# Optimization experiments

Measured on AMD Instinct MI355X. Metric: run time of the kernel, lower is better.

Reference implementation:

```python
import jax, jax.numpy as jnp
import numpy as np

N_NODES = 50000
N_EDGES = 800000
D = 64
N_GRAPHS = 512
N_LAYERS = 3
HID_FC = 64
N_CLASSES = 10


def setup_inputs() -> dict:
    key = jax.random.key(0)
    ks = jax.random.split(key, 12)
    s = 1.0 / np.sqrt(D)
    x = jax.random.normal(ks[0], (N_NODES, D), dtype=jnp.float32)
    edge_index = jax.random.randint(ks[1], (2, N_EDGES), 0, N_NODES, dtype=jnp.int32)
    batch = jnp.sort(jax.random.randint(ks[2], (N_NODES,), 0, N_GRAPHS, dtype=jnp.int32))
    convW1 = jax.random.normal(ks[3], (N_LAYERS, D, D), dtype=jnp.float32) * s
    convb1 = jax.random.normal(ks[4], (N_LAYERS, D), dtype=jnp.float32) * 0.01
    convW2 = jax.random.normal(ks[5], (N_LAYERS, D, D), dtype=jnp.float32) * s
    convb2 = jax.random.normal(ks[6], (N_LAYERS, D), dtype=jnp.float32) * 0.01
    fcW1 = jax.random.normal(ks[7], (D, HID_FC), dtype=jnp.float32) * s
    fcb1 = jax.random.normal(ks[8], (HID_FC,), dtype=jnp.float32) * 0.01
    fcW2 = jax.random.normal(ks[9], (HID_FC, N_CLASSES), dtype=jnp.float32) * (1.0 / np.sqrt(HID_FC))
    fcb2 = jax.random.normal(ks[10], (N_CLASSES,), dtype=jnp.float32) * 0.01
    return {"x": x, "convW1": convW1, "convb1": convb1, "convW2": convW2,
            "convb2": convb2, "fcW1": fcW1, "fcb1": fcb1, "fcW2": fcW2,
            "fcb2": fcb2, "edge_index": edge_index, "batch": batch}


def reference(x, convW1, convb1, convW2, convb2, fcW1, fcb1, fcW2, fcb2, edge_index, batch):
    src, dst = edge_index[0], edge_index[1]
    h = x
    for l in range(N_LAYERS):
        # GIN aggregation: (1 + eps) * x + sum_{j in N(i)} x_j, eps = 0
        agg = jax.ops.segment_sum(h[src], dst, num_segments=N_NODES)
        h = h + agg
        # per-layer MLP: Linear -> ReLU -> Linear
        h = jax.nn.relu(h @ convW1[l] + convb1[l])
        h = h @ convW2[l] + convb2[l]
    # global max pool over nodes of each graph
    g = jax.ops.segment_max(h, batch, num_segments=N_GRAPHS)
    # FC head: Linear(64) -> ReLU -> Linear(num_classes)
    g = jax.nn.relu(g @ fcW1 + fcb1)
    logits = g @ fcW2 + fcb2
    return jax.nn.log_softmax(logits, axis=1)
```

## Files before the change

kernel.cpp:

```cpp
#include <hip/hip_runtime.h>
#include <math.h>

#define N_NODES 50000
#define N_EDGES 800000
#define D 64
#define N_GRAPHS 512
#define N_CLASSES 10
#define NT 3125

#define SCAN_B 512
#define NB_SCAN ((N_NODES + SCAN_B - 1) / SCAN_B)

typedef __attribute__((ext_vector_type(8))) short bf16x8;
typedef __attribute__((ext_vector_type(4))) float f32x4;

#define MFMA16(a, b, c) __builtin_amdgcn_mfma_f32_16x16x32_bf16(a, b, c, 0, 0, 0)


__device__ __forceinline__ unsigned mapf(float f) {
  unsigned u = __float_as_uint(f);
  return (u & 0x80000000u) ? ~u : (u | 0x80000000u);
}
__device__ __forceinline__ float unmapf(unsigned u) {
  return __uint_as_float((u & 0x80000000u) ? (u & 0x7FFFFFFFu) : ~u);
}
__device__ __forceinline__ ushort bf16_rne(float f) {
  unsigned u = __float_as_uint(f);
  u += 0x7FFFu + ((u >> 16) & 1u);
  return (ushort)(u >> 16);
}
__device__ __forceinline__ float bf16_tof(ushort h) {
  return __uint_as_float(((unsigned)h) << 16);
}

__device__ __forceinline__ void split8(float4 p0, float4 p1, bf16x8& H, bf16x8& L) {
  ushort h;
  h = bf16_rne(p0.x); H[0] = (short)h; L[0] = (short)bf16_rne(p0.x - bf16_tof(h));
  h = bf16_rne(p0.y); H[1] = (short)h; L[1] = (short)bf16_rne(p0.y - bf16_tof(h));
  h = bf16_rne(p0.z); H[2] = (short)h; L[2] = (short)bf16_rne(p0.z - bf16_tof(h));
  h = bf16_rne(p0.w); H[3] = (short)h; L[3] = (short)bf16_rne(p0.w - bf16_tof(h));
  h = bf16_rne(p1.x); H[4] = (short)h; L[4] = (short)bf16_rne(p1.x - bf16_tof(h));
  h = bf16_rne(p1.y); H[5] = (short)h; L[5] = (short)bf16_rne(p1.y - bf16_tof(h));
  h = bf16_rne(p1.z); H[6] = (short)h; L[6] = (short)bf16_rne(p1.z - bf16_tof(h));
  h = bf16_rne(p1.w); H[7] = (short)h; L[7] = (short)bf16_rne(p1.w - bf16_tof(h));
}


__global__ void wprep(const float* __restrict__ convW1, const float* __restrict__ convW2,
                      ushort* __restrict__ wf) {
  const int wi = blockIdx.x;
  const int layer = wi >> 1, which = wi & 1;
  const float* W = (which ? convW2 : convW1) + layer * 4096;
  const int t = threadIdx.x;
  const int f = t >> 6, lane = t & 63;
  const int ct = f >> 1, ks = f & 1;
  const int n = ct * 16 + (lane & 15);
  const int k0 = ks * 32 + ((lane >> 4) << 3);
  ushort hi[8], lo[8];
#pragma unroll
  for (int v = 0; v < 8; ++v) {
    float w = W[(k0 + v) * 64 + n];
    ushort h = bf16_rne(w);
    hi[v] = h;
    lo[v] = bf16_rne(w - bf16_tof(h));
  }
  ushort* base = wf + layer * 16384 + which * 8192;
  *(uint4*)(base + f * 512 + lane * 8) = *(uint4*)hi;
  *(uint4*)(base + 4096 + f * 512 + lane * 8) = *(uint4*)lo;
}


__global__ void hist_kernel(const int* __restrict__ dst, int* __restrict__ deg) {
  int e = blockIdx.x * 256 + threadIdx.x;
  if (e < N_EDGES) atomicAdd(&deg[dst[e]], 1);
}

__global__ void scan_blocks(const int* __restrict__ deg, int* __restrict__ bsum) {
  __shared__ int sd[SCAN_B];
  int i = blockIdx.x * SCAN_B + threadIdx.x;
  sd[threadIdx.x] = (i < N_NODES) ? deg[i] : 0;
  __syncthreads();
  for (int off = SCAN_B / 2; off > 0; off >>= 1) {
    if (threadIdx.x < off) sd[threadIdx.x] += sd[threadIdx.x + off];
    __syncthreads();
  }
  if (threadIdx.x == 0) bsum[blockIdx.x] = sd[0];
}

__global__ void scan_mid(int* __restrict__ bsum) {
  __shared__ int s[256];
  int t = threadIdx.x;
  if (t < NB_SCAN) s[t] = bsum[t];
  __syncthreads();
  if (t == 0) {
    int run = 0;
    for (int i = 0; i < NB_SCAN; ++i) { int v = s[i]; s[i] = run; run += v; }
  }
  __syncthreads();
  if (t < NB_SCAN) bsum[t] = s[t];
}

__global__ void scan_final(const int* __restrict__ deg, const int* __restrict__ bsum,
                           int* __restrict__ rs, int* __restrict__ cur) {
  __shared__ int sd[SCAN_B];
  int i = blockIdx.x * SCAN_B + threadIdx.x;
  int v = (i < N_NODES) ? deg[i] : 0;
  sd[threadIdx.x] = v;
  __syncthreads();
  for (int off = 1; off < SCAN_B; off <<= 1) {
    int add = (threadIdx.x >= off) ? sd[threadIdx.x - off] : 0;
    __syncthreads();
    sd[threadIdx.x] += add;
    __syncthreads();
  }
  if (i < N_NODES) {
    int ex = bsum[blockIdx.x] + sd[threadIdx.x] - v;
    rs[i] = ex;
    cur[i] = ex;
  }
  if (i == 0) rs[N_NODES] = N_EDGES;
}

__global__ void fill_csr(const int* __restrict__ src, const int* __restrict__ dst,
                         int* __restrict__ cur, int* __restrict__ csr) {
  int e = blockIdx.x * 256 + threadIdx.x;
  if (e >= N_EDGES) return;
  int p = atomicAdd(&cur[dst[e]], 1);
  csr[p] = src[e];
}


__global__ __launch_bounds__(256) void agg_f32(
    const float* __restrict__ hin, const int* __restrict__ csr,
    const int* __restrict__ rs, float* __restrict__ acc) {
  const int t = threadIdx.x;
  const int hw = t >> 5, hl = t & 31;
  const int node = blockIdx.x * 8 + hw;
  const float2* __restrict__ H = (const float2*)hin;
  float2 a = H[node * 32 + hl];
  int e = rs[node];
  const int e1 = rs[node + 1];
  for (; e + 4 <= e1; e += 4) {
    int s0 = csr[e], s1 = csr[e + 1], s2 = csr[e + 2], s3 = csr[e + 3];
    float2 v0 = H[s0 * 32 + hl];
    float2 v1 = H[s1 * 32 + hl];
    float2 v2 = H[s2 * 32 + hl];
    float2 v3 = H[s3 * 32 + hl];
    a.x += v0.x + v1.x; a.y += v0.y + v1.y;
    a.x += v2.x + v3.x; a.y += v2.y + v3.y;
  }
  for (; e < e1; ++e) {
    float2 v = H[csr[e] * 32 + hl];
    a.x += v.x; a.y += v.y;
  }
  ((float2*)acc)[node * 32 + hl] = a;
}


template <int FINAL>
__global__ __launch_bounds__(256) void mlp_mfma(
    float* __restrict__ A,
    const ushort* __restrict__ wfL,
    const float* __restrict__ b1, const float* __restrict__ b2,
    const int* __restrict__ batch, unsigned* __restrict__ gU) {
  __shared__ char lds[32768 + 4 * 2560];
  const int t = threadIdx.x;
  const int w = t >> 6, lane = t & 63;

  {
    const uint4* s = (const uint4*)wfL;
    uint4* d = (uint4*)lds;
#pragma unroll
    for (int i = 0; i < 8; ++i) d[t + 256 * i] = s[t + 256 * i];
  }
  __syncthreads();

  const int tile = blockIdx.x * 4 + w;
  if (tile >= NT) return;
  const int m = lane & 15, g = lane >> 4;
  const char* wb = lds + lane * 16;
  ushort* tb16 = (ushort*)(lds + 32768 + w * 2560);

  const float* Ar = A + (size_t)(tile * 16 + m) * 64;
  bf16x8 aH0, aH1, aL0, aL1;
  {
    float4 p0 = *(const float4*)(Ar + g * 8);
    float4 p1 = *(const float4*)(Ar + g * 8 + 4);
    float4 p2 = *(const float4*)(Ar + 32 + g * 8);
    float4 p3 = *(const float4*)(Ar + 32 + g * 8 + 4);
    split8(p0, p1, aH0, aL0);
    split8(p2, p3, aH1, aL1);
  }

#define LDW(off) (*(const bf16x8*)(wb + (off)))

  f32x4 c1_0 = {0.f, 0.f, 0.f, 0.f}, c1_1 = c1_0, c1_2 = c1_0, c1_3 = c1_0;
#define G1(ct, cc)                                   \
  cc = MFMA16(aH0, LDW((2 * ct + 0) * 1024), cc);    \
  cc = MFMA16(aH1, LDW((2 * ct + 1) * 1024), cc);    \
  cc = MFMA16(aL0, LDW((2 * ct + 0) * 1024), cc);    \
  cc = MFMA16(aL1, LDW((2 * ct + 1) * 1024), cc);    \
  cc = MFMA16(aH0, LDW(8192 + (2 * ct + 0) * 1024), cc); \
  cc = MFMA16(aH1, LDW(8192 + (2 * ct + 1) * 1024), cc);
  G1(0, c1_0) G1(1, c1_1) G1(2, c1_2) G1(3, c1_3)
#undef G1

  {
    float bv0 = b1[m], bv1 = b1[16 + m], bv2 = b1[32 + m], bv3 = b1[48 + m];
#define BR(cc, bv)                     \
    cc[0] = fmaxf(cc[0] + bv, 0.f);    \
    cc[1] = fmaxf(cc[1] + bv, 0.f);    \
    cc[2] = fmaxf(cc[2] + bv, 0.f);    \
    cc[3] = fmaxf(cc[3] + bv, 0.f);
    BR(c1_0, bv0) BR(c1_1, bv1) BR(c1_2, bv2) BR(c1_3, bv3)
#undef BR
  }

#define WRH(cc, ct)                                                    \
  tb16[(g * 4 + 0) * 80 + ct * 16 + m] = bf16_rne(cc[0]);              \
  tb16[(g * 4 + 1) * 80 + ct * 16 + m] = bf16_rne(cc[1]);              \
  tb16[(g * 4 + 2) * 80 + ct * 16 + m] = bf16_rne(cc[2]);              \
  tb16[(g * 4 + 3) * 80 + ct * 16 + m] = bf16_rne(cc[3]);
  WRH(c1_0, 0) WRH(c1_1, 1) WRH(c1_2, 2) WRH(c1_3, 3)
#undef WRH
  bf16x8 hH0 = *(const bf16x8*)(tb16 + m * 80 + g * 8);
  bf16x8 hH1 = *(const bf16x8*)(tb16 + m * 80 + 32 + g * 8);

#define WRL(cc, ct)                                                                  \
  { float hv; ushort hh;                                                             \
    hv = cc[0]; hh = bf16_rne(hv);                                                   \
    tb16[(g * 4 + 0) * 80 + ct * 16 + m] = bf16_rne(hv - bf16_tof(hh));              \
    hv = cc[1]; hh = bf16_rne(hv);                                                   \
    tb16[(g * 4 + 1) * 80 + ct * 16 + m] = bf16_rne(hv - bf16_tof(hh));              \
    hv = cc[2]; hh = bf16_rne(hv);                                                   \
    tb16[(g * 4 + 2) * 80 + ct * 16 + m] = bf16_rne(hv - bf16_tof(hh));              \
    hv = cc[3]; hh = bf16_rne(hv);                                                   \
    tb16[(g * 4 + 3) * 80 + ct * 16 + m] = bf16_rne(hv - bf16_tof(hh)); }
  WRL(c1_0, 0) WRL(c1_1, 1) WRL(c1_2, 2) WRL(c1_3, 3)
#undef WRL
  bf16x8 hL0 = *(const bf16x8*)(tb16 + m * 80 + g * 8);
  bf16x8 hL1 = *(const bf16x8*)(tb16 + m * 80 + 32 + g * 8);

  f32x4 c2_0 = {0.f, 0.f, 0.f, 0.f}, c2_1 = c2_0, c2_2 = c2_0, c2_3 = c2_0;
#define G2(ct, cc)                                          \
  cc = MFMA16(hH0, LDW(16384 + (2 * ct + 0) * 1024), cc);   \
  cc = MFMA16(hH1, LDW(16384 + (2 * ct + 1) * 1024), cc);   \
  cc = MFMA16(hL0, LDW(16384 + (2 * ct + 0) * 1024), cc);   \
  cc = MFMA16(hL1, LDW(16384 + (2 * ct + 1) * 1024), cc);   \
  cc = MFMA16(hH0, LDW(24576 + (2 * ct + 0) * 1024), cc);   \
  cc = MFMA16(hH1, LDW(24576 + (2 * ct + 1) * 1024), cc);
  G2(0, c2_0) G2(1, c2_1) G2(2, c2_2) G2(3, c2_3)
#undef G2
#undef LDW

  float bv0 = b2[m], bv1 = b2[16 + m], bv2 = b2[32 + m], bv3 = b2[48 + m];
  if (FINAL) {
    int b40 = batch[tile * 16 + g * 4 + 0];
    int b41 = batch[tile * 16 + g * 4 + 1];
    int b42 = batch[tile * 16 + g * 4 + 2];
    int b43 = batch[tile * 16 + g * 4 + 3];
#define PM(cc, ct, bv)                                          \
    atomicMax(&gU[b40 * 64 + ct * 16 + m], mapf(cc[0] + bv));   \
    atomicMax(&gU[b41 * 64 + ct * 16 + m], mapf(cc[1] + bv));   \
    atomicMax(&gU[b42 * 64 + ct * 16 + m], mapf(cc[2] + bv));   \
    atomicMax(&gU[b43 * 64 + ct * 16 + m], mapf(cc[3] + bv));
    PM(c2_0, 0, bv0) PM(c2_1, 1, bv1) PM(c2_2, 2, bv2) PM(c2_3, 3, bv3)
#undef PM
  } else {
    float* Aw = A + (size_t)tile * 1024;
#define ST(cc, ct, bv)                                         \
    Aw[(g * 4 + 0) * 64 + ct * 16 + m] = cc[0] + bv;           \
    Aw[(g * 4 + 1) * 64 + ct * 16 + m] = cc[1] + bv;           \
    Aw[(g * 4 + 2) * 64 + ct * 16 + m] = cc[2] + bv;           \
    Aw[(g * 4 + 3) * 64 + ct * 16 + m] = cc[3] + bv;
    ST(c2_0, 0, bv0) ST(c2_1, 1, bv1) ST(c2_2, 2, bv2) ST(c2_3, 3, bv3)
#undef ST
  }
}


__global__ void init_g(unsigned* __restrict__ gU) {
  int i = blockIdx.x * blockDim.x + threadIdx.x;
  if (i < N_GRAPHS * D) gU[i] = 0x007FFFFFu;
}

__global__ void head_kernel(const unsigned* __restrict__ gU,
                            const float* __restrict__ fcW1, const float* __restrict__ fcb1,
                            const float* __restrict__ fcW2, const float* __restrict__ fcb2,
                            float* __restrict__ out) {
  __shared__ float gbuf[64];
  __shared__ float hid[64];
  __shared__ float logit[N_CLASSES];
  __shared__ float red[2];
  const int gi = blockIdx.x;
  const int t = threadIdx.x;

  gbuf[t] = unmapf(gU[gi * D + t]);
  __syncthreads();

  float a = fcb1[t];
#pragma unroll
  for (int k = 0; k < 64; ++k) a = fmaf(gbuf[k], fcW1[k * 64 + t], a);
  hid[t] = fmaxf(a, 0.0f);
  __syncthreads();

  if (t < N_CLASSES) {
    float l = fcb2[t];
#pragma unroll
    for (int k = 0; k < 64; ++k) l = fmaf(hid[k], fcW2[k * N_CLASSES + t], l);
    logit[t] = l;
  }
  __syncthreads();

  if (t == 0) {
    float mx = logit[0];
    for (int i = 1; i < N_CLASSES; ++i) mx = fmaxf(mx, logit[i]);
    float s = 0.0f;
    for (int i = 0; i < N_CLASSES; ++i) s += expf(logit[i] - mx);
    red[0] = mx;
    red[1] = logf(s);
  }
  __syncthreads();

  if (t < N_CLASSES) out[gi * N_CLASSES + t] = logit[t] - red[0] - red[1];
}


extern "C" void kernel_launch(void* const* d_in, const int* in_sizes, int n_in,
                              void* d_out, int out_size, void* d_ws, size_t ws_size,
                              hipStream_t stream) {
  const float* x      = (const float*)d_in[0];
  const float* convW1 = (const float*)d_in[1];
  const float* convb1 = (const float*)d_in[2];
  const float* convW2 = (const float*)d_in[3];
  const float* convb2 = (const float*)d_in[4];
  const float* fcW1   = (const float*)d_in[5];
  const float* fcb1   = (const float*)d_in[6];
  const float* fcW2   = (const float*)d_in[7];
  const float* fcb2   = (const float*)d_in[8];
  const int*   edge   = (const int*)d_in[9];
  const int*   batch  = (const int*)d_in[10];
  float* out = (float*)d_out;

  const int* src = edge;
  const int* dst = edge + N_EDGES;

  float* accA = (float*)d_ws;
  float* accB = accA + (size_t)N_NODES * 64;
  unsigned* gU = (unsigned*)(accB + (size_t)N_NODES * 64);
  int* rs  = (int*)(gU + N_GRAPHS * D);
  int* csr = rs + N_NODES + 1;
  ushort* wf = (ushort*)(csr + N_EDGES);
  int* deg  = (int*)accA;
  int* cur  = deg + N_NODES;
  int* bsum = cur + N_NODES;

  wprep<<<6, 512, 0, stream>>>(convW1, convW2, wf);
  init_g<<<(N_GRAPHS * D + 255) / 256, 256, 0, stream>>>(gU);

  hipMemsetAsync(deg, 0, N_NODES * sizeof(int), stream);
  hist_kernel<<<N_EDGES / 256, 256, 0, stream>>>(dst, deg);
  scan_blocks<<<NB_SCAN, SCAN_B, 0, stream>>>(deg, bsum);
  scan_mid<<<1, 256, 0, stream>>>(bsum);
  scan_final<<<NB_SCAN, SCAN_B, 0, stream>>>(deg, bsum, rs, cur);
  fill_csr<<<N_EDGES / 256, 256, 0, stream>>>(src, dst, cur, csr);

  const int AGG_B = N_NODES / 8;
  const int MLP_B = (NT + 3) / 4;
  agg_f32<<<AGG_B, 256, 0, stream>>>(x, csr, rs, accA);
  mlp_mfma<0><<<MLP_B, 256, 0, stream>>>(accA, wf, convb1, convb2, batch, gU);
  agg_f32<<<AGG_B, 256, 0, stream>>>(accA, csr, rs, accB);
  mlp_mfma<0><<<MLP_B, 256, 0, stream>>>(accB, wf + 16384, convb1 + 64, convb2 + 64,
                                         batch, gU);
  agg_f32<<<AGG_B, 256, 0, stream>>>(accB, csr, rs, accA);
  mlp_mfma<1><<<MLP_B, 256, 0, stream>>>(accA, wf + 32768, convb1 + 128, convb2 + 128,
                                         batch, gU);

  head_kernel<<<N_GRAPHS, 64, 0, stream>>>(gU, fcW1, fcb1, fcW2, fcb2, out);
}
```

Before: 268.0 us.

## Store node features in bf16 and drop split-precision MFMA passes

Node features are converted to bf16 once, and both aggregation and MLP kernels now read and write bf16 activations, halving gather and store traffic. The MLP drops the hi/lo split compensation, running 4 MFMAs per column tile instead of 6. Weights are staged in LDS one layer-half at a time to cut LDS use and allow more blocks per CU. The cost is accuracy: activations and sums are rounded to bf16 at each layer, which may break the tolerance against the fp32 reference.

```diff
diff --git a/kernel.cpp b/kernel.cpp
--- a/kernel.cpp
+++ b/kernel.cpp
@@ -32,17 +32,18 @@
 __device__ __forceinline__ float bf16_tof(ushort h) {
   return __uint_as_float(((unsigned)h) << 16);
 }
-
-__device__ __forceinline__ void split8(float4 p0, float4 p1, bf16x8& H, bf16x8& L) {
-  ushort h;
-  h = bf16_rne(p0.x); H[0] = (short)h; L[0] = (short)bf16_rne(p0.x - bf16_tof(h));
-  h = bf16_rne(p0.y); H[1] = (short)h; L[1] = (short)bf16_rne(p0.y - bf16_tof(h));
-  h = bf16_rne(p0.z); H[2] = (short)h; L[2] = (short)bf16_rne(p0.z - bf16_tof(h));
-  h = bf16_rne(p0.w); H[3] = (short)h; L[3] = (short)bf16_rne(p0.w - bf16_tof(h));
-  h = bf16_rne(p1.x); H[4] = (short)h; L[4] = (short)bf16_rne(p1.x - bf16_tof(h));
-  h = bf16_rne(p1.y); H[5] = (short)h; L[5] = (short)bf16_rne(p1.y - bf16_tof(h));
-  h = bf16_rne(p1.z); H[6] = (short)h; L[6] = (short)bf16_rne(p1.z - bf16_tof(h));
-  h = bf16_rne(p1.w); H[7] = (short)h; L[7] = (short)bf16_rne(p1.w - bf16_tof(h));
+__device__ __forceinline__ unsigned pack2(float a, float b) {
+  return (unsigned)bf16_rne(a) | ((unsigned)bf16_rne(b) << 16);
+}
+__device__ __forceinline__ float2 unpack2(unsigned v) {
+  return make_float2(__uint_as_float(v << 16), __uint_as_float(v & 0xFFFF0000u));
+}
+
+
+__global__ void to_bf16(const float* __restrict__ in, unsigned* __restrict__ out) {
+  int i = blockIdx.x * 256 + threadIdx.x;
+  float4 v = reinterpret_cast<const float4*>(in)[i];
+  reinterpret_cast<uint2*>(out)[i] = make_uint2(pack2(v.x, v.y), pack2(v.z, v.w));
 }
 
 
@@ -130,151 +131,135 @@
 }
 
 
-__global__ __launch_bounds__(256) void agg_f32(
-    const float* __restrict__ hin, const int* __restrict__ csr,
-    const int* __restrict__ rs, float* __restrict__ acc) {
+__global__ __launch_bounds__(256) void agg_bf16(
+    const unsigned* __restrict__ hin, const int* __restrict__ csr,
+    const int* __restrict__ rs, unsigned* __restrict__ hout) {
   const int t = threadIdx.x;
   const int hw = t >> 5, hl = t & 31;
   const int node = blockIdx.x * 8 + hw;
-  const float2* __restrict__ H = (const float2*)hin;
-  float2 a = H[node * 32 + hl];
+  float2 a = unpack2(hin[node * 32 + hl]);
   int e = rs[node];
   const int e1 = rs[node + 1];
   for (; e + 4 <= e1; e += 4) {
     int s0 = csr[e], s1 = csr[e + 1], s2 = csr[e + 2], s3 = csr[e + 3];
-    float2 v0 = H[s0 * 32 + hl];
-    float2 v1 = H[s1 * 32 + hl];
-    float2 v2 = H[s2 * 32 + hl];
-    float2 v3 = H[s3 * 32 + hl];
+    float2 v0 = unpack2(hin[s0 * 32 + hl]);
+    float2 v1 = unpack2(hin[s1 * 32 + hl]);
+    float2 v2 = unpack2(hin[s2 * 32 + hl]);
+    float2 v3 = unpack2(hin[s3 * 32 + hl]);
     a.x += v0.x + v1.x; a.y += v0.y + v1.y;
     a.x += v2.x + v3.x; a.y += v2.y + v3.y;
   }
   for (; e < e1; ++e) {
-    float2 v = H[csr[e] * 32 + hl];
+    float2 v = unpack2(hin[csr[e] * 32 + hl]);
     a.x += v.x; a.y += v.y;
   }
-  ((float2*)acc)[node * 32 + hl] = a;
+  hout[node * 32 + hl] = pack2(a.x, a.y);
 }
 
 
 template <int FINAL>
-__global__ __launch_bounds__(256) void mlp_mfma(
-    float* __restrict__ A,
+__global__ __launch_bounds__(256, 4) void mlp_bf16(
+    unsigned* __restrict__ A,
     const ushort* __restrict__ wfL,
     const float* __restrict__ b1, const float* __restrict__ b2,
     const int* __restrict__ batch, unsigned* __restrict__ gU) {
-  __shared__ char lds[32768 + 4 * 2560];
+  __shared__ ushort Wl[8192];
+  __shared__ ushort tb[4][16 * 72];
   const int t = threadIdx.x;
   const int w = t >> 6, lane = t & 63;
+  const int tile = blockIdx.x * 4 + w;
+  const bool act = (tile < NT);
+  const int m = lane & 15, g = lane >> 4;
+  ushort* tw = tb[w];
 
   {
     const uint4* s = (const uint4*)wfL;
-    uint4* d = (uint4*)lds;
-#pragma unroll
-    for (int i = 0; i < 8; ++i) d[t + 256 * i] = s[t + 256 * i];
-  }
-  __syncthreads();
-
-  const int tile = blockIdx.x * 4 + w;
-  if (tile >= NT) return;
-  const int m = lane & 15, g = lane >> 4;
-  const char* wb = lds + lane * 16;
-  ushort* tb16 = (ushort*)(lds + 32768 + w * 2560);
-
-  const float* Ar = A + (size_t)(tile * 16 + m) * 64;
-  bf16x8 aH0, aH1, aL0, aL1;
+    uint4* d = (uint4*)Wl;
+#pragma unroll
+    for (int i = 0; i < 4; ++i) d[t + 256 * i] = s[t + 256 * i];
+  }
+
+  bf16x8 a0 = {}, a1 = {};
+  if (act) {
+    const ushort* Ar = (const ushort*)A + (size_t)(tile * 16 + m) * 64;
+    a0 = *(const bf16x8*)(Ar + g * 8);
+    a1 = *(const bf16x8*)(Ar + 32 + g * 8);
+  }
+  __syncthreads();
+
+  const char* wb = (const char*)Wl + lane * 16;
+#define LDW(off) (*(const bf16x8*)(wb + (off)))
+
+  f32x4 c0 = {0.f, 0.f, 0.f, 0.f}, c1 = c0, c2 = c0, c3 = c0;
+  bf16x8 h0 = {}, h1 = {};
+  if (act) {
+#define G1(ct, cc)                                     \
+    cc = MFMA16(a0, LDW((2 * ct + 0) * 1024), cc);     \
+    cc = MFMA16(a1, LDW((2 * ct + 1) * 1024), cc);     \
+    cc = MFMA16(a0, LDW(8192 + (2 * ct + 0) * 1024), cc); \
+    cc = MFMA16(a1, LDW(8192 + (2 * ct + 1) * 1024), cc);
+    G1(0, c0) G1(1, c1) G1(2, c2) G1(3, c3)
+#undef G1
+
+    float bv0 = b1[m], bv1 = b1[16 + m], bv2 = b1[32 + m], bv3 = b1[48 + m];
+#define WRT(cc, ct, bv)                                               \
+    tw[(g * 4 + 0) * 72 + ct * 16 + m] = bf16_rne(fmaxf(cc[0] + bv, 0.f)); \
+    tw[(g * 4 + 1) * 72 + ct * 16 + m] = bf16_rne(fmaxf(cc[1] + bv, 0.f)); \
+    tw[(g * 4 + 2) * 72 + ct * 16 + m] = bf16_rne(fmaxf(cc[2] + bv, 0.f)); \
+    tw[(g * 4 + 3) * 72 + ct * 16 + m] = bf16_rne(fmaxf(cc[3] + bv, 0.f));
+    WRT(c0, 0, bv0) WRT(c1, 1, bv1) WRT(c2, 2, bv2) WRT(c3, 3, bv3)
+#undef WRT
+    h0 = *(const bf16x8*)(tw + m * 72 + g * 8);
+    h1 = *(const bf16x8*)(tw + m * 72 + 32 + g * 8);
+  }
+  __syncthreads();
+
   {
-    float4 p0 = *(const float4*)(Ar + g * 8);
-    float4 p1 = *(const float4*)(Ar + g * 8 + 4);
-    float4 p2 = *(const float4*)(Ar + 32 + g * 8);
-    float4 p3 = *(const float4*)(Ar + 32 + g * 8 + 4);
-    split8(p0, p1, aH0, aL0);
-    split8(p2, p3, aH1, aL1);
-  }
-
-#define LDW(off) (*(const bf16x8*)(wb + (off)))
-
-  f32x4 c1_0 = {0.f, 0.f, 0.f, 0.f}, c1_1 = c1_0, c1_2 = c1_0, c1_3 = c1_0;
-#define G1(ct, cc)                                   \
-  cc = MFMA16(aH0, LDW((2 * ct + 0) * 1024), cc);    \
-  cc = MFMA16(aH1, LDW((2 * ct + 1) * 1024), cc);    \
-  cc = MFMA16(aL0, LDW((2 * ct + 0) * 1024), cc);    \
-  cc = MFMA16(aL1, LDW((2 * ct + 1) * 1024), cc);    \
-  cc = MFMA16(aH0, LDW(8192 + (2 * ct + 0) * 1024), cc); \
-  cc = MFMA16(aH1, LDW(8192 + (2 * ct + 1) * 1024), cc);
-  G1(0, c1_0) G1(1, c1_1) G1(2, c1_2) G1(3, c1_3)
-#undef G1
-
-  {
-    float bv0 = b1[m], bv1 = b1[16 + m], bv2 = b1[32 + m], bv3 = b1[48 + m];
-#define BR(cc, bv)                     \
-    cc[0] = fmaxf(cc[0] + bv, 0.f);    \
-    cc[1] = fmaxf(cc[1] + bv, 0.f);    \
-    cc[2] = fmaxf(cc[2] + bv, 0.f);    \
-    cc[3] = fmaxf(cc[3] + bv, 0.f);
-    BR(c1_0, bv0) BR(c1_1, bv1) BR(c1_2, bv2) BR(c1_3, bv3)
-#undef BR
-  }
-
-#define WRH(cc, ct)                                                    \
-  tb16[(g * 4 + 0) * 80 + ct * 16 + m] = bf16_rne(cc[0]);              \
-  tb16[(g * 4 + 1) * 80 + ct * 16 + m] = bf16_rne(cc[1]);              \
-  tb16[(g * 4 + 2) * 80 + ct * 16 + m] = bf16_rne(cc[2]);              \
-  tb16[(g * 4 + 3) * 80 + ct * 16 + m] = bf16_rne(cc[3]);
-  WRH(c1_0, 0) WRH(c1_1, 1) WRH(c1_2, 2) WRH(c1_3, 3)
-#undef WRH
-  bf16x8 hH0 = *(const bf16x8*)(tb16 + m * 80 + g * 8);
-  bf16x8 hH1 = *(const bf16x8*)(tb16 + m * 80 + 32 + g * 8);
-
-#define WRL(cc, ct)                                                                  \
-  { float hv; ushort hh;                                                             \
-    hv = cc[0]; hh = bf16_rne(hv);                                                   \
-    tb16[(g * 4 + 0) * 80 + ct * 16 + m] = bf16_rne(hv - bf16_tof(hh));              \
-    hv = cc[1]; hh = bf16_rne(hv);                                                   \
-    tb16[(g * 4 + 1) * 80 + ct * 16 + m] = bf16_rne(hv - bf16_tof(hh));              \
-    hv = cc[2]; hh = bf16_rne(hv);                                                   \
-    tb16[(g * 4 + 2) * 80 + ct * 16 + m] = bf16_rne(hv - bf16_tof(hh));              \
-    hv = cc[3]; hh = bf16_rne(hv);                                                   \
-    tb16[(g * 4 + 3) * 80 + ct * 16 + m] = bf16_rne(hv - bf16_tof(hh)); }
-  WRL(c1_0, 0) WRL(c1_1, 1) WRL(c1_2, 2) WRL(c1_3, 3)
-#undef WRL
-  bf16x8 hL0 = *(const bf16x8*)(tb16 + m * 80 + g * 8);
-  bf16x8 hL1 = *(const bf16x8*)(tb16 + m * 80 + 32 + g * 8);
-
-  f32x4 c2_0 = {0.f, 0.f, 0.f, 0.f}, c2_1 = c2_0, c2_2 = c2_0, c2_3 = c2_0;
-#define G2(ct, cc)                                          \
-  cc = MFMA16(hH0, LDW(16384 + (2 * ct + 0) * 1024), cc);   \
-  cc = MFMA16(hH1, LDW(16384 + (2 * ct + 1) * 1024), cc);   \
-  cc = MFMA16(hL0, LDW(16384 + (2 * ct + 0) * 1024), cc);   \
-  cc = MFMA16(hL1, LDW(16384 + (2 * ct + 1) * 1024), cc);   \
-  cc = MFMA16(hH0, LDW(24576 + (2 * ct + 0) * 1024), cc);   \
-  cc = MFMA16(hH1, LDW(24576 + (2 * ct + 1) * 1024), cc);
-  G2(0, c2_0) G2(1, c2_1) G2(2, c2_2) G2(3, c2_3)
+    const uint4* s = (const uint4*)(wfL + 8192);
+    uint4* d = (uint4*)Wl;
+#pragma unroll
+    for (int i = 0; i < 4; ++i) d[t + 256 * i] = s[t + 256 * i];
+  }
+  __syncthreads();
+
+  if (act) {
+    c0 = (f32x4){0.f, 0.f, 0.f, 0.f}; c1 = c0; c2 = c0; c3 = c0;
+#define G2(ct, cc)                                     \
+    cc = MFMA16(h0, LDW((2 * ct + 0) * 1024), cc);     \
+    cc = MFMA16(h1, LDW((2 * ct + 1) * 1024), cc);     \
+    cc = MFMA16(h0, LDW(8192 + (2 * ct + 0) * 1024), cc); \
+    cc = MFMA16(h1, LDW(8192 + (2 * ct + 1) * 1024), cc);
+    G2(0, c0) G2(1, c1) G2(2, c2) G2(3, c3)
 #undef G2
 #undef LDW
 
-  float bv0 = b2[m], bv1 = b2[16 + m], bv2 = b2[32 + m], bv3 = b2[48 + m];
-  if (FINAL) {
-    int b40 = batch[tile * 16 + g * 4 + 0];
-    int b41 = batch[tile * 16 + g * 4 + 1];
-    int b42 = batch[tile * 16 + g * 4 + 2];
-    int b43 = batch[tile * 16 + g * 4 + 3];
+    float bv0 = b2[m], bv1 = b2[16 + m], bv2 = b2[32 + m], bv3 = b2[48 + m];
+    if (FINAL) {
+      int b40 = batch[tile * 16 + g * 4 + 0];
+      int b41 = batch[tile * 16 + g * 4 + 1];
+      int b42 = batch[tile * 16 + g * 4 + 2];
+      int b43 = batch[tile * 16 + g * 4 + 3];
 #define PM(cc, ct, bv)                                          \
-    atomicMax(&gU[b40 * 64 + ct * 16 + m], mapf(cc[0] + bv));   \
-    atomicMax(&gU[b41 * 64 + ct * 16 + m], mapf(cc[1] + bv));   \
-    atomicMax(&gU[b42 * 64 + ct * 16 + m], mapf(cc[2] + bv));   \
-    atomicMax(&gU[b43 * 64 + ct * 16 + m], mapf(cc[3] + bv));
-    PM(c2_0, 0, bv0) PM(c2_1, 1, bv1) PM(c2_2, 2, bv2) PM(c2_3, 3, bv3)
+      atomicMax(&gU[b40 * 64 + ct * 16 + m], mapf(cc[0] + bv)); \
+      atomicMax(&gU[b41 * 64 + ct * 16 + m], mapf(cc[1] + bv)); \
+      atomicMax(&gU[b42 * 64 + ct * 16 + m], mapf(cc[2] + bv)); \
+      atomicMax(&gU[b43 * 64 + ct * 16 + m], mapf(cc[3] + bv));
+      PM(c0, 0, bv0) PM(c1, 1, bv1) PM(c2, 2, bv2) PM(c3, 3, bv3)
 #undef PM
-  } else {
-    float* Aw = A + (size_t)tile * 1024;
-#define ST(cc, ct, bv)                                         \
-    Aw[(g * 4 + 0) * 64 + ct * 16 + m] = cc[0] + bv;           \
-    Aw[(g * 4 + 1) * 64 + ct * 16 + m] = cc[1] + bv;           \
-    Aw[(g * 4 + 2) * 64 + ct * 16 + m] = cc[2] + bv;           \
-    Aw[(g * 4 + 3) * 64 + ct * 16 + m] = cc[3] + bv;
-    ST(c2_0, 0, bv0) ST(c2_1, 1, bv1) ST(c2_2, 2, bv2) ST(c2_3, 3, bv3)
-#undef ST
+    } else {
+#define WRO(cc, ct, bv)                                    \
+      tw[(g * 4 + 0) * 72 + ct * 16 + m] = bf16_rne(cc[0] + bv); \
+      tw[(g * 4 + 1) * 72 + ct * 16 + m] = bf16_rne(cc[1] + bv); \
+      tw[(g * 4 + 2) * 72 + ct * 16 + m] = bf16_rne(cc[2] + bv); \
+      tw[(g * 4 + 3) * 72 + ct * 16 + m] = bf16_rne(cc[3] + bv);
+      WRO(c0, 0, bv0) WRO(c1, 1, bv1) WRO(c2, 2, bv2) WRO(c3, 3, bv3)
+#undef WRO
+      uint4 v0 = *(const uint4*)(tw + m * 72 + g * 16);
+      uint4 v1 = *(const uint4*)(tw + m * 72 + g * 16 + 8);
+      uint4* Aw = (uint4*)((ushort*)A + (size_t)(tile * 16 + m) * 64 + g * 16);
+      Aw[0] = v0;
+      Aw[1] = v1;
+    }
   }
 }
 
@@ -345,16 +330,17 @@
   const int* src = edge;
   const int* dst = edge + N_EDGES;
 
-  float* accA = (float*)d_ws;
-  float* accB = accA + (size_t)N_NODES * 64;
-  unsigned* gU = (unsigned*)(accB + (size_t)N_NODES * 64);
+  unsigned* xb  = (unsigned*)d_ws;
+  unsigned* hbA = xb + (size_t)N_NODES * 32;
+  unsigned* gU  = hbA + (size_t)N_NODES * 32;
   int* rs  = (int*)(gU + N_GRAPHS * D);
   int* csr = rs + N_NODES + 1;
   ushort* wf = (ushort*)(csr + N_EDGES);
-  int* deg  = (int*)accA;
+  int* deg  = (int*)hbA;
   int* cur  = deg + N_NODES;
   int* bsum = cur + N_NODES;
 
+  to_bf16<<<(N_NODES * 16) / 256, 256, 0, stream>>>(x, xb);
   wprep<<<6, 512, 0, stream>>>(convW1, convW2, wf);
   init_g<<<(N_GRAPHS * D + 255) / 256, 256, 0, stream>>>(gU);
 
@@ -367,13 +353,13 @@
 
   const int AGG_B = N_NODES / 8;
   const int MLP_B = (NT + 3) / 4;
-  agg_f32<<<AGG_B, 256, 0, stream>>>(x, csr, rs, accA);
-  mlp_mfma<0><<<MLP_B, 256, 0, stream>>>(accA, wf, convb1, convb2, batch, gU);
-  agg_f32<<<AGG_B, 256, 0, stream>>>(accA, csr, rs, accB);
-  mlp_mfma<0><<<MLP_B, 256, 0, stream>>>(accB, wf + 16384, convb1 + 64, convb2 + 64,
+  agg_bf16<<<AGG_B, 256, 0, stream>>>(xb, csr, rs, hbA);
+  mlp_bf16<0><<<MLP_B, 256, 0, stream>>>(hbA, wf, convb1, convb2, batch, gU);
+  agg_bf16<<<AGG_B, 256, 0, stream>>>(hbA, csr, rs, xb);
+  mlp_bf16<0><<<MLP_B, 256, 0, stream>>>(xb, wf + 16384, convb1 + 64, convb2 + 64,
                                          batch, gU);
-  agg_f32<<<AGG_B, 256, 0, stream>>>(accB, csr, rs, accA);
-  mlp_mfma<1><<<MLP_B, 256, 0, stream>>>(accA, wf + 32768, convb1 + 128, convb2 + 128,
+  agg_bf16<<<AGG_B, 256, 0, stream>>>(xb, csr, rs, hbA);
+  mlp_bf16<1><<<MLP_B, 256, 0, stream>>>(hbA, wf + 32768, convb1 + 128, convb2 + 128,
                                          batch, gU);
 
   head_kernel<<<N_GRAPHS, 64, 0, stream>>>(gU, fcW1, fcb1, fcW2, fcb2, out);
```

New measurement: 242.6 us. -9.5%, faster.
